# Optimization experiments

Measured on AMD Instinct MI355X. Metric: run time of the kernel, lower is better.

Reference implementation:

```python
import jax, jax.numpy as jnp
import numpy as np

N = 60000   # cells
F = 256     # CELL_FEATURE_DIM
H = 128     # HIDDEN_DIM
NH = 8      # NUM_HEADS
DH = H // NH
L = 2       # NUM_LAYERS
C = 256     # tissue clusters
E = 600000  # cell edges
ET = 1500   # tissue edges
NCLS = 4


def _seg_softmax(s, seg, n):
    # numerically stable softmax within segments; s: [E, NH]
    m = jax.ops.segment_max(s, seg, num_segments=n)
    e = jnp.exp(s - m[seg])
    z = jax.ops.segment_sum(e, seg, num_segments=n)
    return e / z[seg]


def _forward(cell_features, cluster_labels, cell_edge_index, tissue_edge_index,
             W_cell_proj, b_cell_proj, W_tissue_proj, b_tissue_proj,
             gat_W, gat_asrc, gat_adst, gat_b, gcn_W, gcn_b,
             bu_Wq, bu_Wk, bu_Wv, bu_bq, bu_bk, bu_bv, bu_Wo, bu_bo,
             td_Wv, td_bv, td_Wo, td_bo,
             gru_Wih, gru_bih, gru_Whh, gru_bhh,
             Wc1, bc1, Wc2, bc2, Wc3, bc3):
    lab = cluster_labels
    # tissue node init = per-cluster mean of raw cell features (as in _construct_tissue_graph)
    cnt = jax.ops.segment_sum(jnp.ones((N,), jnp.float32), lab, num_segments=C)
    tissue_x = jax.ops.segment_sum(cell_features, lab, num_segments=C) / jnp.maximum(cnt, 1.0)[:, None]

    cell_h = cell_features @ W_cell_proj.T + b_cell_proj      # [N, H]
    tissue_h = tissue_x @ W_tissue_proj.T + b_tissue_proj     # [C, H]

    # add self-loops (PyG GATConv / GCNConv default)
    csrc = jnp.concatenate([cell_edge_index[0], jnp.arange(N, dtype=cell_edge_index.dtype)])
    cdst = jnp.concatenate([cell_edge_index[1], jnp.arange(N, dtype=cell_edge_index.dtype)])
    tsrc = jnp.concatenate([tissue_edge_index[0], jnp.arange(C, dtype=tissue_edge_index.dtype)])
    tdst = jnp.concatenate([tissue_edge_index[1], jnp.arange(C, dtype=tissue_edge_index.dtype)])

    # GCN symmetric norm (deg over col, PyG gcn_norm)
    degc = jax.ops.segment_sum(jnp.ones_like(tdst, dtype=jnp.float32), tdst, num_segments=C)
    dinv = jnp.where(degc > 0, 1.0 / jnp.sqrt(degc), 0.0)
    w_e = (dinv[tsrc] * dinv[tdst])[:, None]

    scale = 1.0 / jnp.sqrt(jnp.float32(DH))

    for l in range(L):
        # --- GATConv (multi-head concat) + ELU ---
        h = (cell_h @ gat_W[l].T).reshape(N, NH, DH)
        a_s = (h * gat_asrc[l]).sum(-1)  # [N, NH]
        a_d = (h * gat_adst[l]).sum(-1)
        e = jax.nn.leaky_relu(a_s[csrc] + a_d[cdst], negative_slope=0.2)  # [E+N, NH]
        alpha = _seg_softmax(e, cdst, N)
        agg = jax.ops.segment_sum(h[csrc] * alpha[:, :, None], cdst, num_segments=N)
        cell_h = jax.nn.elu(agg.reshape(N, H) + gat_b[l])

        # --- GCNConv + ReLU on tissue graph ---
        th = tissue_h @ gcn_W[l].T
        tissue_h = jax.nn.relu(jax.ops.segment_sum(th[tsrc] * w_e, tdst, num_segments=C) + gcn_b[l])

        # --- bottom-up cross-level attention: tissue queries attend over their cells ---
        q = ((tissue_h @ bu_Wq.T + bu_bq) * scale).reshape(C, NH, DH)
        k = (cell_h @ bu_Wk.T + bu_bk).reshape(N, NH, DH)
        v = (cell_h @ bu_Wv.T + bu_bv).reshape(N, NH, DH)
        s_att = (q[lab] * k).sum(-1)                       # [N, NH]
        al = _seg_softmax(s_att, lab, C)
        ctx = jax.ops.segment_sum(v * al[:, :, None], lab, num_segments=C).reshape(C, H)
        tissue_h = ctx @ bu_Wo.T + bu_bo

        # --- top-down attention: each cell attends to its single tissue node ---
        # softmax over one key is identically 1, so output = Wo(Wv t + bv) + bo gathered per cell
        td = (tissue_h @ td_Wv.T + td_bv) @ td_Wo.T + td_bo  # [C, H]
        cell_h = td[lab]

        # --- top-down GRUCell refinement: x=[cell;tissue], h=cell ---
        x_in = jnp.concatenate([cell_h, tissue_h[lab]], axis=-1)  # [N, 2H]
        gi = x_in @ gru_Wih.T + gru_bih
        gh = cell_h @ gru_Whh.T + gru_bhh
        r = jax.nn.sigmoid(gi[:, :H] + gh[:, :H])
        z = jax.nn.sigmoid(gi[:, H:2 * H] + gh[:, H:2 * H])
        n = jnp.tanh(gi[:, 2 * H:] + r * gh[:, 2 * H:])
        cell_h = (1.0 - z) * n + z * cell_h

    # dual-pooling readouts (single graph: batch all zeros)
    emb = jnp.concatenate([cell_h.mean(0), cell_h.max(0), tissue_h.mean(0), tissue_h.max(0)])[None, :]  # [1, 4H]
    h1 = jax.nn.relu(emb @ Wc1.T + bc1)
    h2 = jax.nn.relu(h1 @ Wc2.T + bc2)
    return h2 @ Wc3.T + bc3  # [1, NCLS]


def setup_inputs() -> dict:
    k = jax.random.split(jax.random.key(0), 40)
    s = 0.05
    r = lambda i, shape: jax.random.normal(k[i], shape, jnp.float32) * s
    return dict(
        cell_features=jax.random.normal(k[0], (N, F), jnp.float32),
        cell_edge_index=jax.random.randint(k[1], (2, E), 0, N),
        cluster_labels=jax.random.randint(k[2], (N,), 0, C),
        tissue_edge_index=jax.random.randint(k[3], (2, ET), 0, C),
        W_cell_proj=r(4, (H, F)), b_cell_proj=r(5, (H,)),
        W_tissue_proj=r(6, (H, F)), b_tissue_proj=r(7, (H,)),
        gat_W=r(8, (L, H, H)), gat_asrc=r(9, (L, NH, DH)), gat_adst=r(10, (L, NH, DH)), gat_b=r(11, (L, H)),
        gcn_W=r(12, (L, H, H)), gcn_b=r(13, (L, H)),
        bu_Wq=r(14, (H, H)), bu_Wk=r(15, (H, H)), bu_Wv=r(16, (H, H)),
        bu_bq=r(17, (H,)), bu_bk=r(18, (H,)), bu_bv=r(19, (H,)),
        bu_Wo=r(20, (H, H)), bu_bo=r(21, (H,)),
        td_Wv=r(22, (H, H)), td_bv=r(23, (H,)), td_Wo=r(24, (H, H)), td_bo=r(25, (H,)),
        gru_Wih=r(26, (3 * H, 2 * H)), gru_bih=r(27, (3 * H,)),
        gru_Whh=r(28, (3 * H, H)), gru_bhh=r(29, (3 * H,)),
        Wc1=r(30, (2 * H, 4 * H)), bc1=r(31, (2 * H,)),
        Wc2=r(32, (H, 2 * H)), bc2=r(33, (H,)),
        Wc3=r(34, (NCLS, H)), bc3=r(35, (NCLS,)),
    )


def reference(cell_features, cell_edge_index, cluster_labels, tissue_edge_index,
              W_cell_proj, b_cell_proj, W_tissue_proj, b_tissue_proj,
              gat_W, gat_asrc, gat_adst, gat_b, gcn_W, gcn_b,
              bu_Wq, bu_Wk, bu_Wv, bu_bq, bu_bk, bu_bv, bu_Wo, bu_bo,
              td_Wv, td_bv, td_Wo, td_bo,
              gru_Wih, gru_bih, gru_Whh, gru_bhh,
              Wc1, bc1, Wc2, bc2, Wc3, bc3):
    return _forward(cell_features, cluster_labels, cell_edge_index, tissue_edge_index,
                    W_cell_proj, b_cell_proj, W_tissue_proj, b_tissue_proj,
                    gat_W, gat_asrc, gat_adst, gat_b, gcn_W, gcn_b,
                    bu_Wq, bu_Wk, bu_Wv, bu_bq, bu_bk, bu_bv, bu_Wo, bu_bo,
                    td_Wv, td_bv, td_Wo, td_bo,
                    gru_Wih, gru_bih, gru_Whh, gru_bhh,
                    Wc1, bc1, Wc2, bc2, Wc3, bc3)
```

## Files before the change

### kernel.cpp

```cpp
#include <hip/hip_runtime.h>
#include <math.h>

constexpr int N  = 60000;
constexpr int F  = 256;
constexpr int H  = 128;
constexpr int C  = 256;
constexpr int E  = 600000;
constexpr int ET = 1500;
constexpr int NB = (N + 1023) / 1024;
constexpr int SPL = 8;

__global__ void hg_hist(const int* __restrict__ cdst, int* __restrict__ deg,
                        const int* __restrict__ lab, int* __restrict__ ccnt) {
  int e = blockIdx.x * 256 + threadIdx.x;
  if (e < E) atomicAdd(&deg[cdst[e]], 1);
  if (e < N) atomicAdd(&ccnt[lab[e]], 1);
}

__global__ __launch_bounds__(256) void hg_scan1(const int* __restrict__ deg, int* __restrict__ off,
                                                int* __restrict__ btot, int n) {
  int b = blockIdx.x, t = threadIdx.x;
  int i0 = b * 1024 + t * 4;
  __shared__ int sums[256];
  int d0 = 0, d1 = 0, d2 = 0, d3 = 0;
  if (i0 + 3 < n) {
    int4 dd = *(const int4*)&deg[i0];
    d0 = dd.x; d1 = dd.y; d2 = dd.z; d3 = dd.w;
  } else {
    if (i0     < n) d0 = deg[i0];
    if (i0 + 1 < n) d1 = deg[i0 + 1];
    if (i0 + 2 < n) d2 = deg[i0 + 2];
    if (i0 + 3 < n) d3 = deg[i0 + 3];
  }
  int s = d0 + d1 + d2 + d3;
  sums[t] = s;
  __syncthreads();
  for (int ofs = 1; ofs < 256; ofs <<= 1) {
    int v = (t >= ofs) ? sums[t - ofs] : 0;
    __syncthreads();
    sums[t] += v;
    __syncthreads();
  }
  int excl = sums[t] - s;
  if (t == 255) btot[b] = sums[t];
  int run = excl;
  if (i0     < n) off[i0]     = run; run += d0;
  if (i0 + 1 < n) off[i0 + 1] = run; run += d1;
  if (i0 + 2 < n) off[i0 + 2] = run; run += d2;
  if (i0 + 3 < n) off[i0 + 3] = run;
}

__global__ __launch_bounds__(256) void hg_scan2_setup(int* __restrict__ btot, int* __restrict__ off,
                                                      const int* __restrict__ ccnt, int* __restrict__ coff,
                                                      const int* __restrict__ tsrc, const int* __restrict__ tdst,
                                                      int* __restrict__ toff, int* __restrict__ tlist,
                                                      float* __restrict__ dinv) {
  __shared__ int sa[256], sb[256], sc2[256];
  int t = threadIdx.x;
  if (blockIdx.x == 0) {
    if (t < 64) sa[t] = (t < NB) ? btot[t] : 0;
    __syncthreads();
    if (t == 0) {
      int r = 0;
      for (int i = 0; i < NB; ++i) { int v = sa[i]; sa[i] = r; r += v; }
      off[N] = r;
    }
    __syncthreads();
    if (t < NB) btot[t] = sa[t];
  } else if (blockIdx.x == 1) {
    int v0 = ccnt[t];
    sa[t] = v0;
    __syncthreads();
    for (int ofs = 1; ofs < 256; ofs <<= 1) {
      int v = (t >= ofs) ? sa[t - ofs] : 0;
      __syncthreads();
      sa[t] += v;
      __syncthreads();
    }
    coff[t + 1] = sa[t];
    if (t == 0) coff[0] = 0;
  } else {
    sa[t] = 0;
    __syncthreads();
    for (int e = t; e < ET; e += 256) atomicAdd(&sa[tdst[e]], 1);
    __syncthreads();
    int v = sa[t];
    dinv[t] = rsqrtf((float)(v + 1));
    sb[t] = v;
    __syncthreads();
    for (int ofs = 1; ofs < 256; ofs <<= 1) {
      int u = (t >= ofs) ? sb[t - ofs] : 0;
      __syncthreads();
      sb[t] += u;
      __syncthreads();
    }
    toff[t + 1] = sb[t];
    if (t == 0) toff[0] = 0;
    sc2[t] = sb[t] - v;
    __syncthreads();
    for (int e = t; e < ET; e += 256) {
      int d = tdst[e];
      int p = atomicAdd(&sc2[d], 1);
      tlist[p] = tsrc[e];
    }
  }
}

__global__ void hg_scan3(int* __restrict__ off, const int* __restrict__ btot, int n) {
  int b = blockIdx.x;
  int addv = btot[b];
  int i0 = b * 1024 + threadIdx.x * 4;
#pragma unroll
  for (int r = 0; r < 4; ++r)
    if (i0 + r < n) off[i0 + r] += addv;
}

__global__ void hg_scatter(const int* __restrict__ csrc, const int* __restrict__ cdst,
                           const int* __restrict__ off, int* __restrict__ cur, int* __restrict__ csr,
                           const int* __restrict__ lab, const int* __restrict__ coff,
                           int* __restrict__ ccur, int* __restrict__ list) {
  int e = blockIdx.x * 256 + threadIdx.x;
  if (e < E) {
    int d = cdst[e];
    int p = atomicAdd(&cur[d], 1);
    csr[off[d] + p] = csrc[e];
  }
  if (e < N) {
    int c = lab[e];
    int p = atomicAdd(&ccur[c], 1);
    list[coff[c] + p] = e;
  }
}

struct TJob { const float* src; float* dst; int SR; int SC; int dld; };
struct PrepArgs {
  TJob j[8];
  const float* gatW1; const float* Wcp; const float* bcp; float* Wcompt; float* bcomp;
  const float* tdWo; const float* tdWv; const float* tdbv; const float* tdbo;
  float* A_td; float* Wcat_t; float* bcat;
};

__global__ __launch_bounds__(256) void hg_prep1(PrepArgs a) {
  int y = blockIdx.y, t = threadIdx.x;
  if (y < 8) {
    TJob jb = a.j[y];
    int total = jb.SR * jb.SC;
    for (int idx = blockIdx.x * 256 + t; idx < total; idx += gridDim.x * 256) {
      int r = idx / jb.SC, c = idx - r * jb.SC;
      jb.dst[(size_t)c * jb.dld + r] = jb.src[idx];
    }
  } else if (y == 8) {
    int j = blockIdx.x, k = t;
    float acc = 0.f;
#pragma unroll 4
    for (int m = 0; m < 128; ++m) acc = fmaf(a.gatW1[j * 128 + m], a.Wcp[m * 256 + k], acc);
    a.Wcompt[k * 128 + j] = acc;
    if (k == 0) {
      float b = 0.f;
      for (int m = 0; m < 128; ++m) b = fmaf(a.gatW1[j * 128 + m], a.bcp[m], b);
      a.bcomp[j] = b;
    }
  } else if (blockIdx.x < 64) {
    int j = blockIdx.x * 2 + (t >> 7), k = t & 127;
    float acc = 0.f;
#pragma unroll 4
    for (int p = 0; p < 128; ++p) acc = fmaf(a.tdWo[j * 128 + p], a.tdWv[p * 128 + k], acc);
    a.A_td[j * 128 + k] = acc;
    a.Wcat_t[k * 896 + j] = acc;
    if (k == 0) {
      float b = 0.f;
      for (int p = 0; p < 128; ++p) b = fmaf(a.tdWo[j * 128 + p], a.tdbv[p], b);
      a.bcat[j] = b + a.tdbo[j];
    }
  }
}

__global__ __launch_bounds__(256) void hg_pc2b(const float* __restrict__ Wih, const float* __restrict__ bih,
                                               const float* __restrict__ Whh, const float* __restrict__ bhh,
                                               const float* __restrict__ A_td, float* __restrict__ Wcat_t,
                                               float* __restrict__ bcat) {
  int jj = blockIdx.x * 2 + (threadIdx.x >> 7), k = threadIdx.x & 127;
  const float* coef;
  float extra, bb;
  int dcol, j;
  if (jj < 384) {
    j = jj; coef = Wih + (size_t)j * 256; extra = Wih[(size_t)j * 256 + 128 + k]; dcol = 128 + j; bb = bih[j];
  } else {
    j = jj - 384; coef = Whh + (size_t)j * 128; extra = 0.f; dcol = 512 + j; bb = bhh[j];
  }
  float a = 0.f;
#pragma unroll 4
  for (int m = 0; m < 128; ++m) a = fmaf(coef[m], A_td[m * 128 + k], a);
  Wcat_t[k * 896 + dcol] = a + extra;
  if (k == 0) {
    float b = 0.f;
    for (int m = 0; m < 128; ++m) b = fmaf(coef[m], bcat[m], b);
    bcat[dcol] = b + bb;
  }
}

__global__ __launch_bounds__(256, 3) void hg_gemm_coef(
    const float* __restrict__ A, int M, int rtiles,
    const float* __restrict__ Wt, const float* __restrict__ bias,
    float* __restrict__ outp,
    const float* __restrict__ avs, const float* __restrict__ avd,
    float* __restrict__ o_s, float* __restrict__ o_d,
    const int* __restrict__ list, const int* __restrict__ coff,
    const float* __restrict__ Wtpt, const float* __restrict__ btp, float* __restrict__ tish) {
  __shared__ float Al[32][132];
  __shared__ float Wl[32][132];
  const int t = threadIdx.x;

  if (blockIdx.x >= rtiles) {
    int c = blockIdx.x - rtiles;
    float* mrow = (float*)Al;
    int s0 = coff[c], n = coff[c + 1] - s0;
    float acc = 0.f;
#pragma unroll 4
    for (int i = 0; i < n; ++i) acc += A[(size_t)list[s0 + i] * F + t];
    mrow[t] = acc / fmaxf((float)n, 1.f);
    __syncthreads();
    if (t < 128) {
      float a = btp[t];
#pragma unroll 4
      for (int k = 0; k < 256; ++k) a = fmaf(mrow[k], Wtpt[k * 128 + t], a);
      tish[c * 128 + t] = a;
    }
    return;
  }

  const int tx = t & 15, ty = t >> 4;
  const int m0 = blockIdx.x * 128;

  float acc[8][8];
#pragma unroll
  for (int r = 0; r < 8; ++r)
#pragma unroll
    for (int c = 0; c < 8; ++c) acc[r][c] = 0.f;

  const int arow = t & 127, akh = t >> 7;
  const int wkr = t >> 3, wc0 = (t & 7) * 4;
  const int agm = m0 + arow;

  for (int kc = 0; kc < 256; kc += 32) {
#pragma unroll
    for (int f = 0; f < 4; ++f) {
      int k_off = akh * 16 + f * 4;
      float4 a = make_float4(0.f, 0.f, 0.f, 0.f);
      if (agm < M) a = *(const float4*)&A[(size_t)agm * 256 + kc + k_off];
      Al[k_off][arow] = a.x;
      Al[k_off + 1][arow] = a.y;
      Al[k_off + 2][arow] = a.z;
      Al[k_off + 3][arow] = a.w;
    }
#pragma unroll
    for (int f = 0; f < 4; ++f) {
      *(float4*)&Wl[wkr][wc0 + f * 32] = *(const float4*)&Wt[(size_t)(kc + wkr) * 128 + wc0 + f * 32];
    }
    __syncthreads();
#pragma unroll 2
    for (int kk = 0; kk < 32; ++kk) {
      float4 a0 = *(const float4*)&Al[kk][ty * 4];
      float4 a1 = *(const float4*)&Al[kk][64 + ty * 4];
      float4 w0 = *(const float4*)&Wl[kk][tx * 4];
      float4 w1 = *(const float4*)&Wl[kk][64 + tx * 4];
      float ar[8] = {a0.x, a0.y, a0.z, a0.w, a1.x, a1.y, a1.z, a1.w};
      float wr[8] = {w0.x, w0.y, w0.z, w0.w, w1.x, w1.y, w1.z, w1.w};
#pragma unroll
      for (int r = 0; r < 8; ++r)
#pragma unroll
        for (int c = 0; c < 8; ++c) acc[r][c] = fmaf(ar[r], wr[c], acc[r][c]);
    }
    __syncthreads();
  }

  {
    float bA[8];
#pragma unroll
    for (int c = 0; c < 4; ++c) {
      bA[c] = bias[tx * 4 + c];
      bA[4 + c] = bias[64 + tx * 4 + c];
    }
#pragma unroll
    for (int r = 0; r < 8; ++r)
#pragma unroll
      for (int c = 0; c < 8; ++c) acc[r][c] += bA[c];
  }

#pragma unroll
  for (int r = 0; r < 8; ++r) {
    int gm = m0 + ((r < 4) ? (ty * 4 + r) : (64 + ty * 4 + r - 4));
    if (gm < M) {
      float* op = outp + (size_t)gm * 128 + tx * 4;
      *(float4*)op        = make_float4(acc[r][0], acc[r][1], acc[r][2], acc[r][3]);
      *(float4*)(op + 64) = make_float4(acc[r][4], acc[r][5], acc[r][6], acc[r][7]);
    }
  }

  {
    float4 s0 = *(const float4*)&avs[tx * 4], s1 = *(const float4*)&avs[64 + tx * 4];
    float4 d0 = *(const float4*)&avd[tx * 4], d1 = *(const float4*)&avd[64 + tx * 4];
#pragma unroll
    for (int r = 0; r < 8; ++r) {
      int gm = m0 + ((r < 4) ? (ty * 4 + r) : (64 + ty * 4 + r - 4));
      float psA = acc[r][0] * s0.x + acc[r][1] * s0.y + acc[r][2] * s0.z + acc[r][3] * s0.w;
      float psB = acc[r][4] * s1.x + acc[r][5] * s1.y + acc[r][6] * s1.z + acc[r][7] * s1.w;
      float pdA = acc[r][0] * d0.x + acc[r][1] * d0.y + acc[r][2] * d0.z + acc[r][3] * d0.w;
      float pdB = acc[r][4] * d1.x + acc[r][5] * d1.y + acc[r][6] * d1.z + acc[r][7] * d1.w;
      psA += __shfl_xor(psA, 1); psA += __shfl_xor(psA, 2);
      psB += __shfl_xor(psB, 1); psB += __shfl_xor(psB, 2);
      pdA += __shfl_xor(pdA, 1); pdA += __shfl_xor(pdA, 2);
      pdB += __shfl_xor(pdB, 1); pdB += __shfl_xor(pdB, 2);
      if ((tx & 3) == 0 && gm < M) {
        int h = tx >> 2;
        o_s[(size_t)gm * 8 + h] = psA;
        o_s[(size_t)gm * 8 + 4 + h] = psB;
        o_d[(size_t)gm * 8 + h] = pdA;
        o_d[(size_t)gm * 8 + 4 + h] = pdB;
      }
    }
  }
}

#define GMAXE 64
__global__ __launch_bounds__(256) void hg_gat_agg(
    const float* __restrict__ hproj, const float* __restrict__ a_s,
    const float* __restrict__ a_d, const int* __restrict__ remap,
    const int* __restrict__ off, const int* __restrict__ csr,
    const float* __restrict__ bias, float* __restrict__ outh,
    const float* __restrict__ qk, const float* __restrict__ qb,
    const int* __restrict__ lab, const int* __restrict__ nodelist,
    float* __restrict__ satt, int nNodes) {
  const int wid = threadIdx.x >> 6;
  const int l = threadIdx.x & 63;
  const int gid = blockIdx.x * 4 + wid;
  __shared__ int srcs_s[4][GMAXE];
  __shared__ float w_s[4][GMAXE][8];
  if (gid >= nNodes) return;
  const int node = nodelist[gid];
  int* srcs = srcs_s[wid];
  float (*wls)[8] = w_s[wid];
  const int o0 = off[node], deg = off[node + 1] - o0;
  const int cl = lab[node];
  const int dl = remap ? cl : node;
  const int hsc = l & 7;
  const int q4 = l & 31;
  const int sub = l >> 5;
  const int hq = q4 >> 2;
  const float adh = a_d[dl * 8 + hsc];
  const float ash = a_s[dl * 8 + hsc];
  float msc = -INFINITY, zsc = 0.f;
  float4 acc = make_float4(0.f, 0.f, 0.f, 0.f);
  const float4* hp4 = (const float4*)hproj;

  for (int cb = 0; cb < deg; cb += GMAXE) {
    const int len = min(GMAXE, deg - cb);
    if (l < len) {
      int s = csr[o0 + cb + l];
      srcs[l] = remap ? remap[s] : s;
    }
    asm volatile("s_waitcnt lgkmcnt(0)" ::: "memory");
    float lm = -INFINITY;
    for (int base = 0; base < len; base += 8) {
      int e = base + (l >> 3);
      if (e < len) {
        float sc = a_s[srcs[e] * 8 + hsc] + adh;
        sc = sc > 0.f ? sc : 0.2f * sc;
        wls[e][hsc] = sc;
        lm = fmaxf(lm, sc);
      }
    }
    lm = fmaxf(lm, __shfl_xor(lm, 8));
    lm = fmaxf(lm, __shfl_xor(lm, 16));
    lm = fmaxf(lm, __shfl_xor(lm, 32));
    float mnew = fmaxf(msc, lm);
    float rs = __expf(msc - mnew);
    float zc = 0.f;
    asm volatile("s_waitcnt lgkmcnt(0)" ::: "memory");
    for (int base = 0; base < len; base += 8) {
      int e = base + (l >> 3);
      if (e < len) {
        float wv = __expf(wls[e][hsc] - mnew);
        wls[e][hsc] = wv;
        zc += wv;
      }
    }
    asm volatile("s_waitcnt lgkmcnt(0)" ::: "memory");
    zc += __shfl_xor(zc, 8); zc += __shfl_xor(zc, 16); zc += __shfl_xor(zc, 32);
    zsc = zsc * rs + zc;
    msc = mnew;
    float rsa = __shfl(rs, hq);
    acc.x *= rsa; acc.y *= rsa; acc.z *= rsa; acc.w *= rsa;
    for (int e = sub; e < len; e += 2) {
      float wv = wls[e][hq];
      float4 hv = hp4[(size_t)srcs[e] * 32 + q4];
      acc.x = fmaf(wv, hv.x, acc.x);
      acc.y = fmaf(wv, hv.y, acc.y);
      acc.z = fmaf(wv, hv.z, acc.z);
      acc.w = fmaf(wv, hv.w, acc.w);
    }
  }
  float ssl = ash + adh;
  ssl = ssl > 0.f ? ssl : 0.2f * ssl;
  float mnew = fmaxf(msc, ssl);
  float rs = __expf(msc - mnew);
  float wsl = __expf(ssl - mnew);
  zsc = zsc * rs + wsl;
  float rsa = __shfl(rs, hq);
  float wsa = __shfl(wsl, hq);
  float zh = __shfl(zsc, hq);
  acc.x *= rsa; acc.y *= rsa; acc.z *= rsa; acc.w *= rsa;
  acc.x += __shfl_xor(acc.x, 32);
  acc.y += __shfl_xor(acc.y, 32);
  acc.z += __shfl_xor(acc.z, 32);
  acc.w += __shfl_xor(acc.w, 32);
  float4 hv = hp4[(size_t)dl * 32 + q4];
  acc.x = fmaf(wsa, hv.x, acc.x);
  acc.y = fmaf(wsa, hv.y, acc.y);
  acc.z = fmaf(wsa, hv.z, acc.z);
  acc.w = fmaf(wsa, hv.w, acc.w);
  float inv = 1.f / zh;
  float4 bv4 = *(const float4*)&bias[q4 * 4];
  float4 o;
  o.x = acc.x * inv + bv4.x;
  o.y = acc.y * inv + bv4.y;
  o.z = acc.z * inv + bv4.z;
  o.w = acc.w * inv + bv4.w;
  o.x = o.x > 0.f ? o.x : __expf(o.x) - 1.f;
  o.y = o.y > 0.f ? o.y : __expf(o.y) - 1.f;
  o.z = o.z > 0.f ? o.z : __expf(o.z) - 1.f;
  o.w = o.w > 0.f ? o.w : __expf(o.w) - 1.f;
  if (sub == 0) ((float4*)outh)[(size_t)node * 32 + q4] = o;

  const float4* qk4 = (const float4*)(qk + (size_t)cl * 1024);
  float p0, p1, p2, p3;
  {
    float4 qv0 = qk4[(sub * 4 + 0) * 32 + q4];
    float4 qv1 = qk4[(sub * 4 + 1) * 32 + q4];
    float4 qv2 = qk4[(sub * 4 + 2) * 32 + q4];
    float4 qv3 = qk4[(sub * 4 + 3) * 32 + q4];
    p0 = o.x * qv0.x + o.y * qv0.y + o.z * qv0.z + o.w * qv0.w;
    p1 = o.x * qv1.x + o.y * qv1.y + o.z * qv1.z + o.w * qv1.w;
    p2 = o.x * qv2.x + o.y * qv2.y + o.z * qv2.z + o.w * qv2.w;
    p3 = o.x * qv3.x + o.y * qv3.y + o.z * qv3.z + o.w * qv3.w;
  }
  int b4f = (l >> 4) & 1, b3f = (l >> 3) & 1;
  float snd0 = b4f ? p0 : p2, snd1 = b4f ? p1 : p3;
  float kp0  = b4f ? p2 : p0, kp1  = b4f ? p3 : p1;
  kp0 += __shfl_xor(snd0, 16);
  kp1 += __shfl_xor(snd1, 16);
  float snd = b3f ? kp0 : kp1;
  float kp  = b3f ? kp1 : kp0;
  kp += __shfl_xor(snd, 8);
  kp += __shfl_xor(kp, 4);
  kp += __shfl_xor(kp, 2);
  kp += __shfl_xor(kp, 1);
  int h = sub * 4 + b4f * 2 + b3f;
  if ((l & 7) == 0) satt[(size_t)node * 8 + h] = kp + qb[cl * 8 + h];
}

__global__ __launch_bounds__(128) void hg_gcn_q(const float* __restrict__ tin, const int* __restrict__ toff,
                                                const int* __restrict__ tlist, const float* __restrict__ dinv,
                                                const float* __restrict__ gt, const float* __restrict__ gcnb,
                                                const float* __restrict__ Wqt, const float* __restrict__ bq,
                                                const float* __restrict__ Wk, const float* __restrict__ bk,
                                                float* __restrict__ qk, float* __restrict__ qb) {
  int c = blockIdx.x, t = threadIdx.x;
  __shared__ float xa[128], trow[128], qrow[128];
  float dc = dinv[c];
  float acc = tin[c * 128 + t] * dc * dc;
  int s0 = toff[c], s1 = toff[c + 1];
  for (int i = s0; i < s1; ++i) {
    int s = tlist[i];
    acc = fmaf(tin[s * 128 + t], dinv[s] * dc, acc);
  }
  xa[t] = acc;
  __syncthreads();
  float th = 0.f;
#pragma unroll 4
  for (int k = 0; k < 128; ++k) th = fmaf(xa[k], gt[k * 128 + t], th);
  float vv = fmaxf(th + gcnb[t], 0.f);
  trow[t] = vv;
  __syncthreads();
  float qa = bq[t];
#pragma unroll 4
  for (int k = 0; k < 128; ++k) qa = fmaf(trow[k], Wqt[k * 128 + t], qa);
  qrow[t] = qa * 0.25f;
  __syncthreads();
#pragma unroll
  for (int h = 0; h < 8; ++h) {
    float s = 0.f;
#pragma unroll
    for (int j = 0; j < 16; ++j) s = fmaf(Wk[(size_t)(h * 16 + j) * 128 + t], qrow[h * 16 + j], s);
    qk[((size_t)c * 8 + h) * 128 + t] = s;
  }
  if (t < 8) {
    float s = 0.f;
#pragma unroll
    for (int j = 0; j < 16; ++j) s = fmaf(qrow[t * 16 + j], bk[t * 16 + j], s);
    qb[c * 8 + t] = s;
  }
}

__global__ __launch_bounds__(256) void hg_bu_part(
    const float* __restrict__ s_att, const float* __restrict__ hcell,
    const int* __restrict__ list, const int* __restrict__ coff,
    float* __restrict__ pm, float* __restrict__ pz, float* __restrict__ pmacc) {
  int c = blockIdx.x, sp = blockIdx.y, t = threadIdx.x;
  int s0 = coff[c], n = coff[c + 1] - s0;
  int chunk = (n + SPL - 1) / SPL;
  int b0 = min(n, sp * chunk), b1 = min(n, b0 + chunk);
  int cnt = b1 - b0;
  int tf = t & 127, half = t >> 7;
  __shared__ float red[32][8];
  __shared__ float mh[8];
  __shared__ int cells[64];
  __shared__ float wl[64][8];
  __shared__ float msh[8][128];
  int g = t >> 3, h8 = t & 7;
  float lm = -INFINITY;
  for (int i = g; i < cnt; i += 32) lm = fmaxf(lm, s_att[(size_t)list[s0 + b0 + i] * 8 + h8]);
  red[g][h8] = lm;
  __syncthreads();
  if (t < 8) {
    float m2 = -INFINITY;
#pragma unroll
    for (int i = 0; i < 32; ++i) m2 = fmaxf(m2, red[i][t]);
    mh[t] = m2;
  }
  __syncthreads();
  const float mloc = mh[t & 7];
  float zp = 0.f;
  float macc[8] = {0.f, 0.f, 0.f, 0.f, 0.f, 0.f, 0.f, 0.f};
  for (int cb = 0; cb < cnt; cb += 64) {
    int len = min(64, cnt - cb);
    if (t < len) cells[t] = list[s0 + b0 + cb + t];
    __syncthreads();
#pragma unroll
    for (int p = 0; p < 2; ++p) {
      int e = p * 32 + (t >> 3);
      if (e < len) {
        float w = __expf(s_att[(size_t)cells[e] * 8 + (t & 7)] - mloc);
        wl[e][t & 7] = w;
        zp += w;
      }
    }
    __syncthreads();
    for (int e = half; e < len; e += 2) {
      float x = hcell[(size_t)cells[e] * 128 + tf];
      float4 w0 = *(const float4*)&wl[e][0];
      float4 w1 = *(const float4*)&wl[e][4];
      macc[0] = fmaf(w0.x, x, macc[0]);
      macc[1] = fmaf(w0.y, x, macc[1]);
      macc[2] = fmaf(w0.z, x, macc[2]);
      macc[3] = fmaf(w0.w, x, macc[3]);
      macc[4] = fmaf(w1.x, x, macc[4]);
      macc[5] = fmaf(w1.y, x, macc[5]);
      macc[6] = fmaf(w1.z, x, macc[6]);
      macc[7] = fmaf(w1.w, x, macc[7]);
    }
    __syncthreads();
  }
  red[t >> 3][t & 7] = zp;
  __syncthreads();
  int pidx = (c * SPL + sp) * 8;
  if (t < 8) {
    float z = 0.f;
#pragma unroll
    for (int i = 0; i < 32; ++i) z += red[i][t];
    pz[pidx + t] = z;
    pm[pidx + t] = mh[t];
  }
  if (half) {
#pragma unroll
    for (int h = 0; h < 8; ++h) msh[h][tf] = macc[h];
  }
  __syncthreads();
  if (!half) {
#pragma unroll
    for (int h = 0; h < 8; ++h) pmacc[(size_t)(pidx + h) * 128 + tf] = macc[h] + msh[h][tf];
  }
}

__global__ __launch_bounds__(256) void hg_bu_chain(
    const float* __restrict__ pm, const float* __restrict__ pz, const float* __restrict__ pmacc,
    const float* __restrict__ Wv, const float* __restrict__ bv,
    const float* __restrict__ Wot, const float* __restrict__ bo,
    const float* __restrict__ Wcat_t, const float* __restrict__ bcat,
    const float* __restrict__ gatWt, const float* __restrict__ avs, const float* __restrict__ avd,
    float* __restrict__ tish, float* __restrict__ ccell,
    float* __restrict__ hprojc, float* __restrict__ a_s2, float* __restrict__ a_d2) {
  int c = blockIdx.x, t = threadIdx.x;
  int tf = t & 127, half = t >> 7;
  __shared__ float mh[8], zh[8];
  __shared__ float sscale[SPL][8];
  __shared__ float msh[8][128];
  __shared__ float b0[128], b1[128], part[2][128], catv[896];
  const int pbase = c * SPL * 8;
  if (t < 8) {
    float mg = -INFINITY;
#pragma unroll
    for (int s = 0; s < SPL; ++s) mg = fmaxf(mg, pm[pbase + s * 8 + t]);
    mh[t] = mg;
  }
  __syncthreads();
  if (t < SPL * 8) {
    int s = t >> 3, h = t & 7;
    float ms = pm[pbase + s * 8 + h];
    sscale[s][h] = (ms > -1e37f) ? __expf(ms - mh[h]) : 0.f;
  }
  __syncthreads();
  if (t < 8) {
    float z = 0.f;
#pragma unroll
    for (int s = 0; s < SPL; ++s) z += pz[pbase + s * 8 + t] * sscale[s][t];
    zh[t] = (z > 0.f) ? 1.f / z : 0.f;
  }
  __syncthreads();
#pragma unroll
  for (int hh = 0; hh < 4; ++hh) {
    int h = half * 4 + hh;
    float a = 0.f;
#pragma unroll
    for (int s = 0; s < SPL; ++s)
      a = fmaf(pmacc[(size_t)(pbase + s * 8 + h) * 128 + tf], sscale[s][h], a);
    msh[h][tf] = a * zh[h];
  }
  __syncthreads();
  {
    int h = tf >> 4;
    float ps = 0.f;
    const float* wp = Wv + (size_t)tf * 128 + half * 64;
    const float* mp = &msh[h][half * 64];
#pragma unroll 4
    for (int k = 0; k < 64; ++k) ps = fmaf(wp[k], mp[k], ps);
    part[half][tf] = ps;
  }
  __syncthreads();
  if (t < 128) b0[t] = part[0][t] + part[1][t] + bv[t];
  __syncthreads();
  int ks = half;
  {
    float ps = 0.f;
    const float* wp = Wot + (size_t)ks * 64 * 128 + tf;
#pragma unroll 4
    for (int k = 0; k < 64; ++k) ps = fmaf(b0[ks * 64 + k], wp[k * 128], ps);
    part[ks][tf] = ps;
  }
  __syncthreads();
  if (t < 128) {
    float vv = part[0][t] + part[1][t] + bo[t];
    b1[t] = vv;
    tish[c * 128 + t] = vv;
  }
  __syncthreads();
  for (int j = t; j < 896; j += 256) {
    float a = bcat[j];
#pragma unroll 4
    for (int k = 0; k < 128; ++k) a = fmaf(b1[k], Wcat_t[k * 896 + j], a);
    catv[j] = a;
  }
  __syncthreads();
  if (t < 128) {
    float td = catv[t];
    float r = 1.f / (1.f + expf(-(catv[128 + t] + catv[512 + t])));
    float zz = 1.f / (1.f + expf(-(catv[256 + t] + catv[640 + t])));
    float nn = tanhf(catv[384 + t] + r * catv[768 + t]);
    float cn = (1.f - zz) * nn + zz * td;
    ccell[c * 128 + t] = cn;
    b0[t] = cn;
  }
  __syncthreads();
  if (gatWt) {
    float ps = 0.f;
    const float* wp = gatWt + (size_t)ks * 64 * 128 + tf;
#pragma unroll 4
    for (int k = 0; k < 64; ++k) ps = fmaf(b0[ks * 64 + k], wp[k * 128], ps);
    part[ks][tf] = ps;
    __syncthreads();
    if (t < 128) {
      float hp = part[0][t] + part[1][t];
      hprojc[c * 128 + t] = hp;
      float pss = hp * avs[t], pdd = hp * avd[t];
      pss += __shfl_xor(pss, 1); pss += __shfl_xor(pss, 2); pss += __shfl_xor(pss, 4); pss += __shfl_xor(pss, 8);
      pdd += __shfl_xor(pdd, 1); pdd += __shfl_xor(pdd, 2); pdd += __shfl_xor(pdd, 4); pdd += __shfl_xor(pdd, 8);
      if ((t & 15) == 0) {
        a_s2[c * 8 + (t >> 4)] = pss;
        a_d2[c * 8 + (t >> 4)] = pdd;
      }
    }
  }
}

__global__ __launch_bounds__(256) void hg_readout(const float* __restrict__ ccell2, const float* __restrict__ tish,
                                                  const int* __restrict__ cnt, const float* __restrict__ Wc1t,
                                                  const float* __restrict__ bc1, const float* __restrict__ Wc2t,
                                                  const float* __restrict__ bc2, const float* __restrict__ Wc3,
                                                  const float* __restrict__ bc3, float* __restrict__ outp) {
  __shared__ float emb[512], h1s[256], h2s[128];
  int t = threadIdx.x;
  if (t < 128) {
    float sm = 0.f, mx = -INFINITY;
    for (int c = 0; c < C; ++c) {
      float vv = ccell2[c * 128 + t];
      int n = cnt[c];
      sm += (float)n * vv;
      if (n > 0) mx = fmaxf(mx, vv);
    }
    emb[t] = sm / (float)N;
    emb[128 + t] = mx;
  } else {
    int tt = t - 128;
    float sm = 0.f, mx = -INFINITY;
    for (int c = 0; c < C; ++c) {
      float vv = tish[c * 128 + tt];
      sm += vv;
      mx = fmaxf(mx, vv);
    }
    emb[256 + tt] = sm * (1.f / (float)C);
    emb[384 + tt] = mx;
  }
  __syncthreads();
  float a = bc1[t];
#pragma unroll 4
  for (int kk = 0; kk < 512; ++kk) a = fmaf(emb[kk], Wc1t[kk * 256 + t], a);
  h1s[t] = fmaxf(a, 0.f);
  __syncthreads();
  if (t < 128) {
    float a2 = bc2[t];
#pragma unroll 4
    for (int kk = 0; kk < 256; ++kk) a2 = fmaf(h1s[kk], Wc2t[kk * 128 + t], a2);
    h2s[t] = fmaxf(a2, 0.f);
  }
  __syncthreads();
  if (t < 4) {
    float o = bc3[t];
    for (int kk = 0; kk < 128; ++kk) o = fmaf(h2s[kk], Wc3[t * 128 + kk], o);
    outp[t] = o;
  }
}

extern "C" void kernel_launch(void* const* d_in, const int* in_sizes, int n_in,
                              void* d_out, int out_size, void* d_ws, size_t ws_size,
                              hipStream_t stream) {
  (void)in_sizes; (void)n_in; (void)out_size; (void)ws_size;
  const float* feat  = (const float*)d_in[0];
  const int*   eidx  = (const int*)d_in[1];
  const int*   lab   = (const int*)d_in[2];
  const int*   tidx  = (const int*)d_in[3];
  const float* Wcp   = (const float*)d_in[4];
  const float* bcp   = (const float*)d_in[5];
  const float* Wtp   = (const float*)d_in[6];
  const float* btp   = (const float*)d_in[7];
  const float* gatW  = (const float*)d_in[8];
  const float* gasrc = (const float*)d_in[9];
  const float* gadst = (const float*)d_in[10];
  const float* gatb  = (const float*)d_in[11];
  const float* gcnW  = (const float*)d_in[12];
  const float* gcnb  = (const float*)d_in[13];
  const float* buWq  = (const float*)d_in[14];
  const float* buWk  = (const float*)d_in[15];
  const float* buWv  = (const float*)d_in[16];
  const float* bubq  = (const float*)d_in[17];
  const float* bubk  = (const float*)d_in[18];
  const float* bubv  = (const float*)d_in[19];
  const float* buWo  = (const float*)d_in[20];
  const float* bubo  = (const float*)d_in[21];
  const float* tdWv  = (const float*)d_in[22];
  const float* tdbv  = (const float*)d_in[23];
  const float* tdWo  = (const float*)d_in[24];
  const float* tdbo  = (const float*)d_in[25];
  const float* Wih   = (const float*)d_in[26];
  const float* bih   = (const float*)d_in[27];
  const float* Whh   = (const float*)d_in[28];
  const float* bhh   = (const float*)d_in[29];
  const float* Wc1   = (const float*)d_in[30];
  const float* bc1   = (const float*)d_in[31];
  const float* Wc2   = (const float*)d_in[32];
  const float* bc2   = (const float*)d_in[33];
  const float* Wc3   = (const float*)d_in[34];
  const float* bc3   = (const float*)d_in[35];
  float* outp = (float*)d_out;

  const int* csrc = eidx;
  const int* cdst = eidx + E;
  const int* tsrc = tidx;
  const int* tdst = tidx + ET;

  char* w = (char*)d_ws;
  auto alloc = [&](size_t bytes) -> void* {
    void* p = (void*)w;
    w += (bytes + 255) & ~(size_t)255;
    return p;
  };
  char* cnt0 = w;
  int* deg_cell = (int*)alloc((size_t)N * 4);
  int* cur_cell = (int*)alloc((size_t)N * 4);
  int* clu_cnt  = (int*)alloc((size_t)C * 4);
  int* clu_cur  = (int*)alloc((size_t)C * 4);
  size_t cntBytes = (size_t)(w - cnt0);
  int* off_cell = (int*)alloc((size_t)(N + 1) * 4);
  int* btot     = (int*)alloc(64 * 4);
  int* csr      = (int*)alloc((size_t)E * 4);
  int* clu_off  = (int*)alloc((size_t)(C + 1) * 4);
  int* clu_list = (int*)alloc((size_t)N * 4);
  int* toff     = (int*)alloc((size_t)(C + 1) * 4);
  int* tlist    = (int*)alloc((size_t)ET * 4);
  float* dinv   = (float*)alloc((size_t)C * 4);
  float* buf1   = (float*)alloc((size_t)N * 128 * 4);
  float* buf2   = (float*)alloc((size_t)N * 128 * 4);
  float* a_s    = (float*)alloc((size_t)N * 8 * 4);
  float* a_d    = (float*)alloc((size_t)N * 8 * 4);
  float* s_att  = (float*)alloc((size_t)N * 8 * 4);
  float* tish   = (float*)alloc((size_t)C * 128 * 4);
  float* qkb    = (float*)alloc((size_t)C * 8 * 128 * 4);
  float* qbb    = (float*)alloc((size_t)C * 8 * 4);
  float* ccell  = (float*)alloc((size_t)C * 128 * 4);
  float* hprojc = (float*)alloc((size_t)C * 128 * 4);
  float* a_sc   = (float*)alloc((size_t)C * 8 * 4);
  float* a_dc   = (float*)alloc((size_t)C * 8 * 4);
  float* pm     = (float*)alloc((size_t)C * SPL * 8 * 4);
  float* pz     = (float*)alloc((size_t)C * SPL * 8 * 4);
  float* pmacc  = (float*)alloc((size_t)C * SPL * 8 * 128 * 4);
  float* A_td   = (float*)alloc(128 * 128 * 4);
  float* Wcat_t = (float*)alloc(128 * 896 * 4);
  float* bcat   = (float*)alloc(896 * 4);
  float* Wcompt = (float*)alloc(256 * 128 * 4);
  float* bcomp  = (float*)alloc(128 * 4);
  float* Wtpt   = (float*)alloc(256 * 128 * 4);
  float* g1t    = (float*)alloc(128 * 128 * 4);
  float* g2t    = (float*)alloc(128 * 128 * 4);
  float* Wqt    = (float*)alloc(128 * 128 * 4);
  float* Wot    = (float*)alloc(128 * 128 * 4);
  float* gatW2t = (float*)alloc(128 * 128 * 4);
  float* Wc1t   = (float*)alloc(512 * 256 * 4);
  float* Wc2t   = (float*)alloc(256 * 128 * 4);

  hipMemsetAsync(cnt0, 0, cntBytes, stream);

  hg_hist<<<(E + 255) / 256, 256, 0, stream>>>(cdst, deg_cell, lab, clu_cnt);
  hg_scan1<<<NB, 256, 0, stream>>>(deg_cell, off_cell, btot, N);
  hg_scan2_setup<<<3, 256, 0, stream>>>(btot, off_cell, clu_cnt, clu_off, tsrc, tdst, toff, tlist, dinv);
  hg_scan3<<<NB, 256, 0, stream>>>(off_cell, btot, N);
  hg_scatter<<<(E + 255) / 256, 256, 0, stream>>>(csrc, cdst, off_cell, cur_cell, csr,
                                                  lab, clu_off, clu_cur, clu_list);

  PrepArgs pa;
  pa.j[0] = {Wtp,            Wtpt,   128, 256, 128};
  pa.j[1] = {gcnW,           g1t,    128, 128, 128};
  pa.j[2] = {gcnW + 128*128, g2t,    128, 128, 128};
  pa.j[3] = {buWq,           Wqt,    128, 128, 128};
  pa.j[4] = {buWo,           Wot,    128, 128, 128};
  pa.j[5] = {gatW + 128*128, gatW2t, 128, 128, 128};
  pa.j[6] = {Wc1,            Wc1t,   256, 512, 256};
  pa.j[7] = {Wc2,            Wc2t,   128, 256, 128};
  pa.gatW1 = gatW; pa.Wcp = Wcp; pa.bcp = bcp; pa.Wcompt = Wcompt; pa.bcomp = bcomp;
  pa.tdWo = tdWo; pa.tdWv = tdWv; pa.tdbv = tdbv; pa.tdbo = tdbo;
  pa.A_td = A_td; pa.Wcat_t = Wcat_t; pa.bcat = bcat;
  hg_prep1<<<dim3(128, 10), 256, 0, stream>>>(pa);
  hg_pc2b<<<384, 256, 0, stream>>>(Wih, bih, Whh, bhh, A_td, Wcat_t, bcat);

  const int RT = (N + 127) / 128;
  hg_gemm_coef<<<RT + C, 256, 0, stream>>>(feat, N, RT, Wcompt, bcomp, buf2, gasrc, gadst, a_s, a_d,
                                           clu_list, clu_off, Wtpt, btp, tish);
  hg_gcn_q<<<C, 128, 0, stream>>>(tish, toff, tlist, dinv, g1t, gcnb, Wqt, bubq, buWk, bubk, qkb, qbb);
  hg_gat_agg<<<(N + 3) / 4, 256, 0, stream>>>(buf2, a_s, a_d, nullptr, off_cell, csr, gatb, buf1,
                                              qkb, qbb, lab, clu_list, s_att, N);
  hg_bu_part<<<dim3(C, SPL), 256, 0, stream>>>(s_att, buf1, clu_list, clu_off, pm, pz, pmacc);
  hg_bu_chain<<<C, 256, 0, stream>>>(pm, pz, pmacc, buWv, bubv, Wot, bubo, Wcat_t, bcat,
                                     gatW2t, gasrc + 128, gadst + 128, tish, ccell, hprojc, a_sc, a_dc);
  hg_gcn_q<<<C, 128, 0, stream>>>(tish, toff, tlist, dinv, g2t, gcnb + 128, Wqt, bubq, buWk, bubk, qkb, qbb);
  hg_gat_agg<<<(N + 3) / 4, 256, 0, stream>>>(hprojc, a_sc, a_dc, lab, off_cell, csr, gatb + 128, buf1,
                                              qkb, qbb, lab, clu_list, s_att, N);
  hg_bu_part<<<dim3(C, SPL), 256, 0, stream>>>(s_att, buf1, clu_list, clu_off, pm, pz, pmacc);
  hg_bu_chain<<<C, 256, 0, stream>>>(pm, pz, pmacc, buWv, bubv, Wot, bubo, Wcat_t, bcat,
                                     nullptr, nullptr, nullptr, tish, ccell, nullptr, nullptr, nullptr);

  hg_readout<<<1, 256, 0, stream>>>(ccell, tish, clu_cnt, Wc1t, bc1, Wc2t, bc2, Wc3, bc3, outp);
}
```

Measured before the change: 570.3 us.

## Use bf16 MFMA for cell projection GEMM and store hidden features in bf16

Replaces the FP32 LDS-tiled SIMT GEMM for the fused cell projection with bf16 MFMA 16x16x32 instructions, converting activations to bf16 on the fly and precomputing the combined weight in bf16. The projected hidden features, the GAT outputs and the tissue projection buffers are now stored as bf16, which halves the bytes moved by the gather-heavy GAT aggregation and bottom-up partial kernels. This adds rounding error from bf16 storage and bf16 matmul inputs, and removes LDS staging, so A and B operands are read straight from global memory.

After: 555.4 us. 2.6% less time.

```diff
diff --git a/kernel.cpp b/kernel.cpp
--- a/kernel.cpp
+++ b/kernel.cpp
@@ -9,6 +9,17 @@
 constexpr int ET = 1500;
 constexpr int NB = (N + 1023) / 1024;
 constexpr int SPL = 8;
+
+typedef __attribute__((ext_vector_type(8))) short short8;
+typedef __attribute__((ext_vector_type(4))) float f32x4;
+
+__device__ __forceinline__ unsigned short f2b(float f) {
+  unsigned int u = __float_as_uint(f);
+  return (unsigned short)((u + 0x7FFFu + ((u >> 16) & 1u)) >> 16);
+}
+__device__ __forceinline__ float b2f(unsigned short b) {
+  return __uint_as_float(((unsigned int)b) << 16);
+}
 
 __global__ void hg_hist(const int* __restrict__ cdst, int* __restrict__ deg,
                         const int* __restrict__ lab, int* __restrict__ ccnt) {
@@ -135,7 +146,7 @@
 struct TJob { const float* src; float* dst; int SR; int SC; int dld; };
 struct PrepArgs {
   TJob j[8];
-  const float* gatW1; const float* Wcp; const float* bcp; float* Wcompt; float* bcomp;
+  const float* gatW1; const float* Wcp; const float* bcp; short* Wcompb; float* bcomp;
   const float* tdWo; const float* tdWv; const float* tdbv; const float* tdbo;
   float* A_td; float* Wcat_t; float* bcat;
 };
@@ -154,7 +165,7 @@
     float acc = 0.f;
 #pragma unroll 4
     for (int m = 0; m < 128; ++m) acc = fmaf(a.gatW1[j * 128 + m], a.Wcp[m * 256 + k], acc);
-    a.Wcompt[k * 128 + j] = acc;
+    a.Wcompb[(size_t)j * 256 + k] = (short)f2b(acc);
     if (k == 0) {
       float b = 0.f;
       for (int m = 0; m < 128; ++m) b = fmaf(a.gatW1[j * 128 + m], a.bcp[m], b);
@@ -199,21 +210,20 @@
   }
 }
 
-__global__ __launch_bounds__(256, 3) void hg_gemm_coef(
+__global__ __launch_bounds__(256, 2) void hg_gemm_coef(
     const float* __restrict__ A, int M, int rtiles,
-    const float* __restrict__ Wt, const float* __restrict__ bias,
-    float* __restrict__ outp,
+    const short* __restrict__ Wb,
+    const float* __restrict__ bias,
+    unsigned short* __restrict__ outp,
     const float* __restrict__ avs, const float* __restrict__ avd,
     float* __restrict__ o_s, float* __restrict__ o_d,
     const int* __restrict__ list, const int* __restrict__ coff,
     const float* __restrict__ Wtpt, const float* __restrict__ btp, float* __restrict__ tish) {
-  __shared__ float Al[32][132];
-  __shared__ float Wl[32][132];
+  __shared__ float mrow[256];
   const int t = threadIdx.x;
 
   if (blockIdx.x >= rtiles) {
     int c = blockIdx.x - rtiles;
-    float* mrow = (float*)Al;
     int s0 = coff[c], n = coff[c + 1] - s0;
     float acc = 0.f;
 #pragma unroll 4
@@ -229,94 +239,67 @@
     return;
   }
 
-  const int tx = t & 15, ty = t >> 4;
-  const int m0 = blockIdx.x * 128;
-
-  float acc[8][8];
-#pragma unroll
-  for (int r = 0; r < 8; ++r)
-#pragma unroll
-    for (int c = 0; c < 8; ++c) acc[r][c] = 0.f;
-
-  const int arow = t & 127, akh = t >> 7;
-  const int wkr = t >> 3, wc0 = (t & 7) * 4;
-  const int agm = m0 + arow;
+  const int w = t >> 6, l = t & 63;
+  const int li = l & 15, lk = l >> 4;
+  const int m0 = blockIdx.x * 128 + w * 32;
+
+  f32x4 zero = {0.f, 0.f, 0.f, 0.f};
+  f32x4 acc[2][8];
+#pragma unroll
+  for (int rt = 0; rt < 2; ++rt)
+#pragma unroll
+    for (int ct = 0; ct < 8; ++ct) acc[rt][ct] = zero;
+
+  const int r0 = m0 + li, r1 = m0 + 16 + li;
+  const bool v0 = r0 < M, v1 = r1 < M;
+  const float* a0p = A + (size_t)r0 * 256 + lk * 8;
+  const float* a1p = A + (size_t)r1 * 256 + lk * 8;
 
   for (int kc = 0; kc < 256; kc += 32) {
-#pragma unroll
-    for (int f = 0; f < 4; ++f) {
-      int k_off = akh * 16 + f * 4;
-      float4 a = make_float4(0.f, 0.f, 0.f, 0.f);
-      if (agm < M) a = *(const float4*)&A[(size_t)agm * 256 + kc + k_off];
-      Al[k_off][arow] = a.x;
-      Al[k_off + 1][arow] = a.y;
-      Al[k_off + 2][arow] = a.z;
-      Al[k_off + 3][arow] = a.w;
-    }
-#pragma unroll
-    for (int f = 0; f < 4; ++f) {
-      *(float4*)&Wl[wkr][wc0 + f * 32] = *(const float4*)&Wt[(size_t)(kc + wkr) * 128 + wc0 + f * 32];
-    }
-    __syncthreads();
-#pragma unroll 2
-    for (int kk = 0; kk < 32; ++kk) {
-      float4 a0 = *(const float4*)&Al[kk][ty * 4];
-      float4 a1 = *(const float4*)&Al[kk][64 + ty * 4];
-      float4 w0 = *(const float4*)&Wl[kk][tx * 4];
-      float4 w1 = *(const float4*)&Wl[kk][64 + tx * 4];
-      float ar[8] = {a0.x, a0.y, a0.z, a0.w, a1.x, a1.y, a1.z, a1.w};
-      float wr[8] = {w0.x, w0.y, w0.z, w0.w, w1.x, w1.y, w1.z, w1.w};
-#pragma unroll
-      for (int r = 0; r < 8; ++r)
-#pragma unroll
-        for (int c = 0; c < 8; ++c) acc[r][c] = fmaf(ar[r], wr[c], acc[r][c]);
-    }
-    __syncthreads();
-  }
-
-  {
-    float bA[8];
-#pragma unroll
-    for (int c = 0; c < 4; ++c) {
-      bA[c] = bias[tx * 4 + c];
-      bA[4 + c] = bias[64 + tx * 4 + c];
-    }
-#pragma unroll
-    for (int r = 0; r < 8; ++r)
-#pragma unroll
-      for (int c = 0; c < 8; ++c) acc[r][c] += bA[c];
-  }
-
-#pragma unroll
-  for (int r = 0; r < 8; ++r) {
-    int gm = m0 + ((r < 4) ? (ty * 4 + r) : (64 + ty * 4 + r - 4));
-    if (gm < M) {
-      float* op = outp + (size_t)gm * 128 + tx * 4;
-      *(float4*)op        = make_float4(acc[r][0], acc[r][1], acc[r][2], acc[r][3]);
-      *(float4*)(op + 64) = make_float4(acc[r][4], acc[r][5], acc[r][6], acc[r][7]);
-    }
-  }
-
-  {
-    float4 s0 = *(const float4*)&avs[tx * 4], s1 = *(const float4*)&avs[64 + tx * 4];
-    float4 d0 = *(const float4*)&avd[tx * 4], d1 = *(const float4*)&avd[64 + tx * 4];
-#pragma unroll
-    for (int r = 0; r < 8; ++r) {
-      int gm = m0 + ((r < 4) ? (ty * 4 + r) : (64 + ty * 4 + r - 4));
-      float psA = acc[r][0] * s0.x + acc[r][1] * s0.y + acc[r][2] * s0.z + acc[r][3] * s0.w;
-      float psB = acc[r][4] * s1.x + acc[r][5] * s1.y + acc[r][6] * s1.z + acc[r][7] * s1.w;
-      float pdA = acc[r][0] * d0.x + acc[r][1] * d0.y + acc[r][2] * d0.z + acc[r][3] * d0.w;
-      float pdB = acc[r][4] * d1.x + acc[r][5] * d1.y + acc[r][6] * d1.z + acc[r][7] * d1.w;
-      psA += __shfl_xor(psA, 1); psA += __shfl_xor(psA, 2);
-      psB += __shfl_xor(psB, 1); psB += __shfl_xor(psB, 2);
-      pdA += __shfl_xor(pdA, 1); pdA += __shfl_xor(pdA, 2);
-      pdB += __shfl_xor(pdB, 1); pdB += __shfl_xor(pdB, 2);
-      if ((tx & 3) == 0 && gm < M) {
-        int h = tx >> 2;
-        o_s[(size_t)gm * 8 + h] = psA;
-        o_s[(size_t)gm * 8 + 4 + h] = psB;
-        o_d[(size_t)gm * 8 + h] = pdA;
-        o_d[(size_t)gm * 8 + 4 + h] = pdB;
+    short8 bf[8];
+#pragma unroll
+    for (int ct = 0; ct < 8; ++ct)
+      bf[ct] = *(const short8*)&Wb[(size_t)(ct * 16 + li) * 256 + kc + lk * 8];
+    short8 af0 = {0, 0, 0, 0, 0, 0, 0, 0};
+    short8 af1 = {0, 0, 0, 0, 0, 0, 0, 0};
+    if (v0) {
+      float4 x = *(const float4*)(a0p + kc);
+      float4 y = *(const float4*)(a0p + kc + 4);
+      af0[0] = (short)f2b(x.x); af0[1] = (short)f2b(x.y); af0[2] = (short)f2b(x.z); af0[3] = (short)f2b(x.w);
+      af0[4] = (short)f2b(y.x); af0[5] = (short)f2b(y.y); af0[6] = (short)f2b(y.z); af0[7] = (short)f2b(y.w);
+    }
+    if (v1) {
+      float4 x = *(const float4*)(a1p + kc);
+      float4 y = *(const float4*)(a1p + kc + 4);
+      af1[0] = (short)f2b(x.x); af1[1] = (short)f2b(x.y); af1[2] = (short)f2b(x.z); af1[3] = (short)f2b(x.w);
+      af1[4] = (short)f2b(y.x); af1[5] = (short)f2b(y.y); af1[6] = (short)f2b(y.z); af1[7] = (short)f2b(y.w);
+    }
+#pragma unroll
+    for (int ct = 0; ct < 8; ++ct) {
+      acc[0][ct] = __builtin_amdgcn_mfma_f32_16x16x32_bf16(af0, bf[ct], acc[0][ct], 0, 0, 0);
+      acc[1][ct] = __builtin_amdgcn_mfma_f32_16x16x32_bf16(af1, bf[ct], acc[1][ct], 0, 0, 0);
+    }
+  }
+
+#pragma unroll
+  for (int ct = 0; ct < 8; ++ct) {
+    float bj = bias[ct * 16 + li];
+    float as = avs[ct * 16 + li];
+    float ad = avd[ct * 16 + li];
+#pragma unroll
+    for (int rt = 0; rt < 2; ++rt) {
+#pragma unroll
+      for (int r = 0; r < 4; ++r) {
+        int gm = m0 + rt * 16 + lk * 4 + r;
+        float v = acc[rt][ct][r] + bj;
+        if (gm < M) outp[(size_t)gm * 128 + ct * 16 + li] = f2b(v);
+        float ps = v * as, pd = v * ad;
+        ps += __shfl_xor(ps, 1); ps += __shfl_xor(ps, 2); ps += __shfl_xor(ps, 4); ps += __shfl_xor(ps, 8);
+        pd += __shfl_xor(pd, 1); pd += __shfl_xor(pd, 2); pd += __shfl_xor(pd, 4); pd += __shfl_xor(pd, 8);
+        if (li == 0 && gm < M) {
+          o_s[(size_t)gm * 8 + ct] = ps;
+          o_d[(size_t)gm * 8 + ct] = pd;
+        }
       }
     }
   }
@@ -324,10 +307,10 @@
 
 #define GMAXE 64
 __global__ __launch_bounds__(256) void hg_gat_agg(
-    const float* __restrict__ hproj, const float* __restrict__ a_s,
+    const unsigned short* __restrict__ hproj, const float* __restrict__ a_s,
     const float* __restrict__ a_d, const int* __restrict__ remap,
     const int* __restrict__ off, const int* __restrict__ csr,
-    const float* __restrict__ bias, float* __restrict__ outh,
+    const float* __restrict__ bias, unsigned short* __restrict__ outh,
     const float* __restrict__ qk, const float* __restrict__ qb,
     const int* __restrict__ lab, const int* __restrict__ nodelist,
     float* __restrict__ satt, int nNodes) {
@@ -351,7 +334,7 @@
   const float ash = a_s[dl * 8 + hsc];
   float msc = -INFINITY, zsc = 0.f;
   float4 acc = make_float4(0.f, 0.f, 0.f, 0.f);
-  const float4* hp4 = (const float4*)hproj;
+  const ushort4* hp4 = (const ushort4*)hproj;
 
   for (int cb = 0; cb < deg; cb += GMAXE) {
     const int len = min(GMAXE, deg - cb);
@@ -393,11 +376,11 @@
     acc.x *= rsa; acc.y *= rsa; acc.z *= rsa; acc.w *= rsa;
     for (int e = sub; e < len; e += 2) {
       float wv = wls[e][hq];
-      float4 hv = hp4[(size_t)srcs[e] * 32 + q4];
-      acc.x = fmaf(wv, hv.x, acc.x);
-      acc.y = fmaf(wv, hv.y, acc.y);
-      acc.z = fmaf(wv, hv.z, acc.z);
-      acc.w = fmaf(wv, hv.w, acc.w);
+      ushort4 hv = hp4[(size_t)srcs[e] * 32 + q4];
+      acc.x = fmaf(wv, b2f(hv.x), acc.x);
+      acc.y = fmaf(wv, b2f(hv.y), acc.y);
+      acc.z = fmaf(wv, b2f(hv.z), acc.z);
+      acc.w = fmaf(wv, b2f(hv.w), acc.w);
     }
   }
   float ssl = ash + adh;
@@ -414,11 +397,11 @@
   acc.y += __shfl_xor(acc.y, 32);
   acc.z += __shfl_xor(acc.z, 32);
   acc.w += __shfl_xor(acc.w, 32);
-  float4 hv = hp4[(size_t)dl * 32 + q4];
-  acc.x = fmaf(wsa, hv.x, acc.x);
-  acc.y = fmaf(wsa, hv.y, acc.y);
-  acc.z = fmaf(wsa, hv.z, acc.z);
-  acc.w = fmaf(wsa, hv.w, acc.w);
+  ushort4 hvs = hp4[(size_t)dl * 32 + q4];
+  acc.x = fmaf(wsa, b2f(hvs.x), acc.x);
+  acc.y = fmaf(wsa, b2f(hvs.y), acc.y);
+  acc.z = fmaf(wsa, b2f(hvs.z), acc.z);
+  acc.w = fmaf(wsa, b2f(hvs.w), acc.w);
   float inv = 1.f / zh;
   float4 bv4 = *(const float4*)&bias[q4 * 4];
   float4 o;
@@ -430,7 +413,10 @@
   o.y = o.y > 0.f ? o.y : __expf(o.y) - 1.f;
   o.z = o.z > 0.f ? o.z : __expf(o.z) - 1.f;
   o.w = o.w > 0.f ? o.w : __expf(o.w) - 1.f;
-  if (sub == 0) ((float4*)outh)[(size_t)node * 32 + q4] = o;
+  if (sub == 0) {
+    ushort4 ov = make_ushort4(f2b(o.x), f2b(o.y), f2b(o.z), f2b(o.w));
+    ((ushort4*)outh)[(size_t)node * 32 + q4] = ov;
+  }
 
   const float4* qk4 = (const float4*)(qk + (size_t)cl * 1024);
   float p0, p1, p2, p3;
@@ -503,7 +489,7 @@
 }
 
 __global__ __launch_bounds__(256) void hg_bu_part(
-    const float* __restrict__ s_att, const float* __restrict__ hcell,
+    const float* __restrict__ s_att, const unsigned short* __restrict__ hcell,
     const int* __restrict__ list, const int* __restrict__ coff,
     float* __restrict__ pm, float* __restrict__ pz, float* __restrict__ pmacc) {
   int c = blockIdx.x, sp = blockIdx.y, t = threadIdx.x;
@@ -547,7 +533,7 @@
     }
     __syncthreads();
     for (int e = half; e < len; e += 2) {
-      float x = hcell[(size_t)cells[e] * 128 + tf];
+      float x = b2f(hcell[(size_t)cells[e] * 128 + tf]);
       float4 w0 = *(const float4*)&wl[e][0];
       float4 w1 = *(const float4*)&wl[e][4];
       macc[0] = fmaf(w0.x, x, macc[0]);
@@ -589,7 +575,7 @@
     const float* __restrict__ Wcat_t, const float* __restrict__ bcat,
     const float* __restrict__ gatWt, const float* __restrict__ avs, const float* __restrict__ avd,
     float* __restrict__ tish, float* __restrict__ ccell,
-    float* __restrict__ hprojc, float* __restrict__ a_s2, float* __restrict__ a_d2) {
+    unsigned short* __restrict__ hprojc, float* __restrict__ a_s2, float* __restrict__ a_d2) {
   int c = blockIdx.x, t = threadIdx.x;
   int tf = t & 127, half = t >> 7;
   __shared__ float mh[8], zh[8];
@@ -680,7 +666,7 @@
     __syncthreads();
     if (t < 128) {
       float hp = part[0][t] + part[1][t];
-      hprojc[c * 128 + t] = hp;
+      hprojc[c * 128 + t] = f2b(hp);
       float pss = hp * avs[t], pdd = hp * avd[t];
       pss += __shfl_xor(pss, 1); pss += __shfl_xor(pss, 2); pss += __shfl_xor(pss, 4); pss += __shfl_xor(pss, 8);
       pdd += __shfl_xor(pdd, 1); pdd += __shfl_xor(pdd, 2); pdd += __shfl_xor(pdd, 4); pdd += __shfl_xor(pdd, 8);
@@ -807,8 +793,8 @@
   int* toff     = (int*)alloc((size_t)(C + 1) * 4);
   int* tlist    = (int*)alloc((size_t)ET * 4);
   float* dinv   = (float*)alloc((size_t)C * 4);
-  float* buf1   = (float*)alloc((size_t)N * 128 * 4);
-  float* buf2   = (float*)alloc((size_t)N * 128 * 4);
+  unsigned short* buf1 = (unsigned short*)alloc((size_t)N * 128 * 2);
+  unsigned short* buf2 = (unsigned short*)alloc((size_t)N * 128 * 2);
   float* a_s    = (float*)alloc((size_t)N * 8 * 4);
   float* a_d    = (float*)alloc((size_t)N * 8 * 4);
   float* s_att  = (float*)alloc((size_t)N * 8 * 4);
@@ -816,7 +802,7 @@
   float* qkb    = (float*)alloc((size_t)C * 8 * 128 * 4);
   float* qbb    = (float*)alloc((size_t)C * 8 * 4);
   float* ccell  = (float*)alloc((size_t)C * 128 * 4);
-  float* hprojc = (float*)alloc((size_t)C * 128 * 4);
+  unsigned short* hprojc = (unsigned short*)alloc((size_t)C * 128 * 2);
   float* a_sc   = (float*)alloc((size_t)C * 8 * 4);
   float* a_dc   = (float*)alloc((size_t)C * 8 * 4);
   float* pm     = (float*)alloc((size_t)C * SPL * 8 * 4);
@@ -825,7 +811,7 @@
   float* A_td   = (float*)alloc(128 * 128 * 4);
   float* Wcat_t = (float*)alloc(128 * 896 * 4);
   float* bcat   = (float*)alloc(896 * 4);
-  float* Wcompt = (float*)alloc(256 * 128 * 4);
+  short* Wcompb = (short*)alloc(128 * 256 * 2);
   float* bcomp  = (float*)alloc(128 * 4);
   float* Wtpt   = (float*)alloc(256 * 128 * 4);
   float* g1t    = (float*)alloc(128 * 128 * 4);
@@ -854,14 +840,14 @@
   pa.j[5] = {gatW + 128*128, gatW2t, 128, 128, 128};
   pa.j[6] = {Wc1,            Wc1t,   256, 512, 256};
   pa.j[7] = {Wc2,            Wc2t,   128, 256, 128};
-  pa.gatW1 = gatW; pa.Wcp = Wcp; pa.bcp = bcp; pa.Wcompt = Wcompt; pa.bcomp = bcomp;
+  pa.gatW1 = gatW; pa.Wcp = Wcp; pa.bcp = bcp; pa.Wcompb = Wcompb; pa.bcomp = bcomp;
   pa.tdWo = tdWo; pa.tdWv = tdWv; pa.tdbv = tdbv; pa.tdbo = tdbo;
   pa.A_td = A_td; pa.Wcat_t = Wcat_t; pa.bcat = bcat;
   hg_prep1<<<dim3(128, 10), 256, 0, stream>>>(pa);
   hg_pc2b<<<384, 256, 0, stream>>>(Wih, bih, Whh, bhh, A_td, Wcat_t, bcat);
 
   const int RT = (N + 127) / 128;
-  hg_gemm_coef<<<RT + C, 256, 0, stream>>>(feat, N, RT, Wcompt, bcomp, buf2, gasrc, gadst, a_s, a_d,
+  hg_gemm_coef<<<RT + C, 256, 0, stream>>>(feat, N, RT, Wcompb, bcomp, buf2, gasrc, gadst, a_s, a_d,
                                            clu_list, clu_off, Wtpt, btp, tish);
   hg_gcn_q<<<C, 128, 0, stream>>>(tish, toff, tlist, dinv, g1t, gcnb, Wqt, bubq, buWk, bubk, qkb, qbb);
   hg_gat_agg<<<(N + 3) / 4, 256, 0, stream>>>(buf2, a_s, a_d, nullptr, off_cell, csr, gatb, buf1,
```
